# Optimization experiments

Measured on AMD Instinct MI355X. Metric: run time of the kernel, lower is better.

Reference implementation:

```python
import math
import jax, jax.numpy as jnp
import numpy as np

B, T, C, FD, K, V = 8, 2048, 256, 256, 128, 256

def setup_inputs() -> dict:
    key = jax.random.key(0)
    ks = jax.random.split(key, 8)
    s = 0.02
    return {
        "inp": jax.random.normal(ks[0], (B, T, C), jnp.float32),
        "feature": jax.random.normal(ks[1], (B, T, FD), jnp.float32),
        "Wq": jax.random.normal(ks[2], (C + FD, K), jnp.float32) * s,
        "bq": jnp.zeros((K,), jnp.float32),
        "Wk": jax.random.normal(ks[3], (C, K), jnp.float32) * s,
        "bk": jnp.zeros((K,), jnp.float32),
        "Wv": jax.random.normal(ks[4], (C, V), jnp.float32) * s,
        "bv": jnp.zeros((V,), jnp.float32),
    }

def reference(inp, feature, Wq, bq, Wk, bk, Wv, bv):
    # inp: [B,T,C], feature: [B,T,FD]
    t = inp.shape[1]
    q = jnp.concatenate([inp, feature], axis=-1) @ Wq + bq   # [B,T,K]
    k = inp @ Wk + bk                                        # [B,T,K]
    v = inp @ Wv + bv                                        # [B,T,V]
    # scores[b, j, i] = q_j . k_i ; original masks where i > j (strict upper tri)
    scores = jnp.einsum('bjk,bik->bji', q, k)                # [B,T,T]
    mask = jnp.triu(jnp.ones((t, t), dtype=bool), k=1)       # mask[j,i] = i > j
    scores = jnp.where(mask[None], -jnp.inf, scores) / math.sqrt(K)
    # NOTE: original softmax is over dim=1 (the query/row axis), not the key axis
    attn = jax.nn.softmax(scores, axis=1)                    # [B,T,T]
    out = jnp.einsum('bji,biv->bjv', attn, v)                # [B,T,V]
    return jnp.concatenate([inp, out], axis=-1)              # [B,T,C+V]
```

## Files before the change

kernel.cpp:

```cpp
#include <hip/hip_runtime.h>
#include <hip/hip_bf16.h>
#include <cstdint>

#define Bb  8
#define Tt  2048
#define Cc  256
#define FDd 256
#define Kk  128
#define Vv  256
#define BT  (Bb * Tt)
#define NTRI 136

#define INV_SQRT_K 0.08838834764831845f

typedef __bf16 bf16x8 __attribute__((ext_vector_type(8)));
typedef __bf16 bf16x4 __attribute__((ext_vector_type(4)));
typedef float  f32x4  __attribute__((ext_vector_type(4)));

__device__ __forceinline__ void gload16(const void* g, void* l) {
  __builtin_amdgcn_global_load_lds(
      (const __attribute__((address_space(1))) void*)g,
      (__attribute__((address_space(3))) void*)l, 16, 0, 0);
}

__global__ __launch_bounds__(256) void prepw_kernel(
    const float4* __restrict__ inp4, const float4* __restrict__ feat4,
    float4* __restrict__ out4, bf16x4* __restrict__ inpB4,
    bf16x4* __restrict__ featB4,
    const float* __restrict__ Wq, const float* __restrict__ Wk,
    const float* __restrict__ Wv, __bf16* __restrict__ Wqt,
    __bf16* __restrict__ Wkt, __bf16* __restrict__ Wvt)
{
  if (blockIdx.x < 4096) {
    const int g = blockIdx.x * 256 + threadIdx.x;
    const int row = g >> 6, c = g & 63;
    const float4 x = inp4[g];
    out4[(size_t)row * 128 + c] = x;
    bf16x4 xb; xb[0] = (__bf16)x.x; xb[1] = (__bf16)x.y; xb[2] = (__bf16)x.z; xb[3] = (__bf16)x.w;
    inpB4[g] = xb;
    const float4 f = feat4[g];
    bf16x4 fb; fb[0] = (__bf16)f.x; fb[1] = (__bf16)f.y; fb[2] = (__bf16)f.z; fb[3] = (__bf16)f.w;
    featB4[g] = fb;
  } else {
    const int g = (blockIdx.x - 4096) * 256 + threadIdx.x;
    if (g < 65536) {
      const int n = g >> 9, k = g & 511;
      Wqt[g] = (__bf16)Wq[k * 128 + n];
    } else if (g < 98304) {
      const int h = g - 65536;
      const int n = h >> 8, k = h & 255;
      Wkt[h] = (__bf16)Wk[k * 128 + n];
    } else {
      const int h = g - 98304;
      const int n = h >> 8, k = h & 255;
      Wvt[h] = (__bf16)Wv[k * 256 + n];
    }
  }
}

__global__ __launch_bounds__(256, 3) void qkv_mfma_kernel(
    const __bf16* __restrict__ inpB, const __bf16* __restrict__ featB,
    const __bf16* __restrict__ Wqt, const __bf16* __restrict__ Wkt,
    const __bf16* __restrict__ Wvt,
    const float* __restrict__ bq, const float* __restrict__ bk,
    const float* __restrict__ bv,
    __bf16* __restrict__ qb, __bf16* __restrict__ kb, __bf16* __restrict__ vT)
{
  __shared__ __bf16 Atile[128 * 64];
  __shared__ __bf16 Btile[128 * 64];
  const int panel = blockIdx.y;
  const int m0 = blockIdx.x * 128;
  const int lane = threadIdx.x & 63, wave = threadIdx.x >> 6;
  const int cl = lane & 15, quad = lane >> 4;
  const int jl0 = (wave >> 1) * 64;
  const int vl0 = (wave & 1) * 64;

  const __bf16* Wt; const float* bias; int kblocks;
  if (panel == 0)      { Wt = Wqt; bias = bq; kblocks = 8; }
  else if (panel == 1) { Wt = Wkt; bias = bk; kblocks = 4; }
  else                 { Wt = Wvt + (size_t)(panel - 2) * 128 * 256;
                         bias = bv + (panel - 2) * 128; kblocks = 4; }
  const int Kd = kblocks * 64;

  const int lrow = lane >> 3;
  const int lchunk = ((lane & 7) ^ lrow) * 8;

  f32x4 acc[4][4];
#pragma unroll
  for (int mt = 0; mt < 4; ++mt)
#pragma unroll
    for (int nt = 0; nt < 4; ++nt) acc[mt][nt] = (f32x4){0.f, 0.f, 0.f, 0.f};

  for (int kb = 0; kb < kblocks; ++kb) {
    const __bf16* Asrc = (panel == 0 && kb >= 4) ? featB : inpB;
    const int koff = (panel == 0 && kb >= 4) ? (kb - 4) * 64 : kb * 64;
    __syncthreads();
#pragma unroll
    for (int t = 0; t < 4; ++t) {
      const int r0 = wave * 32 + t * 8;
      gload16(Asrc + (size_t)(m0 + r0 + lrow) * 256 + koff + lchunk, Atile + r0 * 64);
      gload16(Wt + (size_t)(r0 + lrow) * Kd + kb * 64 + lchunk, Btile + r0 * 64);
    }
    __syncthreads();
#pragma unroll
    for (int ks = 0; ks < 2; ++ks) {
      bf16x8 af[4], bfr[4];
#pragma unroll
      for (int mt = 0; mt < 4; ++mt) {
        const int jlr = jl0 + mt * 16 + cl;
        af[mt] = *(const bf16x8*)(Atile + jlr * 64 + (((ks * 4 + quad) ^ (jlr & 7)) * 8));
      }
#pragma unroll
      for (int nt = 0; nt < 4; ++nt) {
        const int vlr = vl0 + nt * 16 + cl;
        bfr[nt] = *(const bf16x8*)(Btile + vlr * 64 + (((ks * 4 + quad) ^ (vlr & 7)) * 8));
      }
#pragma unroll
      for (int mt = 0; mt < 4; ++mt)
#pragma unroll
        for (int nt = 0; nt < 4; ++nt)
          acc[mt][nt] = __builtin_amdgcn_mfma_f32_16x16x32_bf16(af[mt], bfr[nt], acc[mt][nt], 0, 0, 0);
    }
  }

  if (panel < 2) {
    __bf16* dst = (panel == 0) ? qb : kb;
    const float scale = (panel == 0) ? INV_SQRT_K : 1.0f;
#pragma unroll
    for (int mt = 0; mt < 4; ++mt) {
      const int row = m0 + jl0 + mt * 16 + quad * 4;
#pragma unroll
      for (int nt = 0; nt < 4; ++nt) {
        const int col = vl0 + nt * 16 + cl;
        const float bs = bias[col];
#pragma unroll
        for (int r = 0; r < 4; ++r)
          dst[(size_t)(row + r) * Kk + col] = (__bf16)((acc[mt][nt][r] + bs) * scale);
      }
    }
  } else {
    const int b = m0 >> 11;
#pragma unroll
    for (int mt = 0; mt < 4; ++mt) {
      const int t0 = (m0 & (Tt - 1)) + jl0 + mt * 16 + quad * 4;
#pragma unroll
      for (int nt = 0; nt < 4; ++nt) {
        const int vcol = (panel - 2) * 128 + vl0 + nt * 16 + cl;
        const float bs = bias[vl0 + nt * 16 + cl];
        bf16x4 v4;
#pragma unroll
        for (int r = 0; r < 4; ++r) v4[r] = (__bf16)(acc[mt][nt][r] + bs);
        *(bf16x4*)(vT + (size_t)(b * Vv + vcol) * Tt + t0) = v4;
      }
    }
  }
}

__global__ __launch_bounds__(256, 2) void sexp_kernel(
    const __bf16* __restrict__ qb, const __bf16* __restrict__ kb,
    __bf16* __restrict__ expS, float* __restrict__ partialD)
{
  __shared__ __bf16 tiles[2 * 128 * 128];
  __shared__ float lcs[4][64];
  __bf16* Qtile = tiles;
  __bf16* Ktile = tiles + 128 * 128;
  float*  P     = (float*)tiles;

  const int b = blockIdx.x, l = blockIdx.y;
  int jt = 0, base = 0;
  while (base + jt + 1 <= l) { base += jt + 1; ++jt; }
  const int it = l - base;

  const int lane = threadIdx.x & 63, wave = threadIdx.x >> 6;
  const int cl = lane & 15, quad = lane >> 4;
  const int jl0 = (wave >> 1) * 64;
  const int il0 = (wave & 1) * 64;
  const size_t rowbase = (size_t)b * Tt;

  {
    const int srow = lane >> 4;
    const int cslot = lane & 15;
    const __bf16* qsrc = qb + (rowbase + jt * 128) * Kk;
    const __bf16* ksrc = kb + (rowbase + it * 128) * Kk;
#pragma unroll
    for (int t = 0; t < 8; ++t) {
      const int r0 = wave * 32 + t * 4;
      const int row = r0 + srow;
      const int cg = (cslot ^ (row & 7)) * 8;
      gload16(qsrc + (size_t)row * Kk + cg, Qtile + r0 * 128);
      gload16(ksrc + (size_t)row * Kk + cg, Ktile + r0 * 128);
    }
  }
  __syncthreads();

  f32x4 acc[4][4];
#pragma unroll
  for (int mt = 0; mt < 4; ++mt)
#pragma unroll
    for (int nt = 0; nt < 4; ++nt) acc[mt][nt] = (f32x4){0.f, 0.f, 0.f, 0.f};

#pragma unroll
  for (int s = 0; s < 4; ++s) {
    bf16x8 af[4], bfr[4];
#pragma unroll
    for (int mt = 0; mt < 4; ++mt) {
      const int jlr = jl0 + mt * 16 + cl;
      af[mt] = *(const bf16x8*)(Qtile + jlr * 128 + (((s * 4 + quad) ^ (jlr & 7)) * 8));
    }
#pragma unroll
    for (int nt = 0; nt < 4; ++nt) {
      const int ilr = il0 + nt * 16 + cl;
      bfr[nt] = *(const bf16x8*)(Ktile + ilr * 128 + (((s * 4 + quad) ^ (ilr & 7)) * 8));
    }
#pragma unroll
    for (int mt = 0; mt < 4; ++mt)
#pragma unroll
      for (int nt = 0; nt < 4; ++nt)
        acc[mt][nt] = __builtin_amdgcn_mfma_f32_16x16x32_bf16(af[mt], bfr[nt], acc[mt][nt], 0, 0, 0);
  }
  __syncthreads();

  const bool diag = (it == jt);
  float cs[4] = {0.f, 0.f, 0.f, 0.f};
#pragma unroll
  for (int mt = 0; mt < 4; ++mt) {
    const int jl = jl0 + mt * 16 + quad * 4;
#pragma unroll
    for (int nt = 0; nt < 4; ++nt) {
      const int il = il0 + nt * 16 + cl;
#pragma unroll
      for (int r = 0; r < 4; ++r) {
        float p = __expf(acc[mt][nt][r]);
        if (diag && il > (jl + r)) p = 0.f;
        cs[nt] += (float)(__bf16)p;
        const int row = jl + r;
        P[row * 128 + (il ^ (((row >> 2) & 1) << 4))] = p;
      }
    }
  }
#pragma unroll
  for (int nt = 0; nt < 4; ++nt) {
    cs[nt] += __shfl_xor(cs[nt], 16);
    cs[nt] += __shfl_xor(cs[nt], 32);
  }
  if (quad == 0) {
#pragma unroll
    for (int nt = 0; nt < 4; ++nt) lcs[wave][nt * 16 + cl] = cs[nt];
  }
  __syncthreads();

  __bf16* slot = expS + ((size_t)(b * NTRI + l)) * (128 * 128);
  {
    const int srow = lane >> 4;
    const int c0 = (lane & 15) * 8;
#pragma unroll
    for (int t = 0; t < 8; ++t) {
      const int row = wave * 32 + t * 4 + srow;
      const int c0p = c0 ^ (((row >> 2) & 1) << 4);
      const f32x4 p0 = *(const f32x4*)(P + row * 128 + c0p);
      const f32x4 p1 = *(const f32x4*)(P + row * 128 + c0p + 4);
      bf16x8 pb;
#pragma unroll
      for (int u = 0; u < 4; ++u) { pb[u] = (__bf16)p0[u]; pb[4 + u] = (__bf16)p1[u]; }
      *(bf16x8*)(slot + (size_t)row * 128 + c0) = pb;
    }
  }

  const int tid = threadIdx.x;
  if (tid < 128) {
    const int w0 = (tid < 64) ? 0 : 1;
    const int lc = tid & 63;
    const float s = lcs[w0][lc] + lcs[w0 + 2][lc];
    partialD[((size_t)b * 16 + jt) * Tt + it * 128 + tid] = s;
  }
}

__global__ __launch_bounds__(256) void dvscale_kernel(
    const float* __restrict__ partialD, bf16x8* __restrict__ vT8)
{
  __shared__ float rec[32];
  const int b = blockIdx.x, ic = blockIdx.y;
  const int i0 = ic * 32;
  const int tid = threadIdx.x;
  if (tid < 32) {
    const int i = i0 + tid;
    float s = 0.f;
#pragma unroll
    for (int jt = 0; jt < 16; ++jt) s += partialD[((size_t)b * 16 + jt) * Tt + i];
    rec[tid] = 1.0f / s;
  }
  __syncthreads();
  const int iu = tid & 3, v0 = tid >> 2;
#pragma unroll
  for (int p = 0; p < 4; ++p) {
    const int v = v0 + p * 64;
    const size_t idx = ((size_t)b * Vv + v) * (Tt / 8) + (i0 >> 3) + iu;
    bf16x8 x = vT8[idx];
    const int rb = iu * 8;
#pragma unroll
    for (int t = 0; t < 8; ++t) x[t] = (__bf16)((float)x[t] * rec[rb + t]);
    vT8[idx] = x;
  }
}

__global__ __launch_bounds__(256, 4) void pvgemm_kernel(
    const __bf16* __restrict__ expS, const __bf16* __restrict__ vT,
    float* __restrict__ out)
{
  __shared__ __bf16 At[2][64 * 64];
  __shared__ __bf16 Bt[2][64 * 64];
  const int b = blockIdx.x;
  const int p = blockIdx.y >> 2;
  const int nq = blockIdx.y & 3;
  const int lane = threadIdx.x & 63, wave = threadIdx.x >> 6;
  const int cl = lane & 15, quad = lane >> 4;
  const int jl0 = (wave >> 1) * 32;
  const int vl0 = (wave & 1) * 32;
  const int lrow = lane >> 3;
  const int lchunk = ((lane & 7) ^ lrow) * 8;
  const __bf16* vbase = vT + ((size_t)b * Vv + nq * 64) * Tt;

#pragma unroll
  for (int sp = 0; sp < 2; ++sp) {
    const int jt64 = sp ? p : 31 - p;
    const int jt128 = jt64 >> 1;
    const int rowoff = (jt64 & 1) * 64;
    const int ksteps = jt64 + 1;
    const size_t tribase = (size_t)(b * NTRI + (jt128 * (jt128 + 1)) / 2) * 16384;

    f32x4 acc[2][2];
#pragma unroll
    for (int mt = 0; mt < 2; ++mt)
#pragma unroll
      for (int nt = 0; nt < 2; ++nt) acc[mt][nt] = (f32x4){0.f, 0.f, 0.f, 0.f};

#pragma unroll
    for (int t = 0; t < 2; ++t) {
      const int r0 = wave * 16 + t * 8;
      gload16(expS + tribase + (size_t)(rowoff + r0 + lrow) * 128 + lchunk,
              At[0] + r0 * 64);
      gload16(vbase + (size_t)(r0 + lrow) * Tt + lchunk, Bt[0] + r0 * 64);
    }
    __syncthreads();

    int buf = 0;
    for (int kb = 0; kb < ksteps; ++kb) {
      if (kb + 1 < ksteps) {
        const int kn = kb + 1;
        const __bf16* Ag = expS + tribase + (size_t)(kn >> 1) * 16384
                         + (size_t)rowoff * 128 + (kn & 1) * 64;
        const int i0n = kn * 64;
#pragma unroll
        for (int t = 0; t < 2; ++t) {
          const int r0 = wave * 16 + t * 8;
          gload16(Ag + (size_t)(r0 + lrow) * 128 + lchunk, At[buf ^ 1] + r0 * 64);
          gload16(vbase + (size_t)(r0 + lrow) * Tt + i0n + lchunk, Bt[buf ^ 1] + r0 * 64);
        }
      }
#pragma unroll
      for (int ks = 0; ks < 2; ++ks) {
        bf16x8 af[2], bfr[2];
#pragma unroll
        for (int mt = 0; mt < 2; ++mt) {
          const int jlr = jl0 + mt * 16 + cl;
          af[mt] = *(const bf16x8*)(At[buf] + jlr * 64 + (((ks * 4 + quad) ^ (jlr & 7)) * 8));
        }
#pragma unroll
        for (int nt = 0; nt < 2; ++nt) {
          const int vlr = vl0 + nt * 16 + cl;
          bfr[nt] = *(const bf16x8*)(Bt[buf] + vlr * 64 + (((ks * 4 + quad) ^ (vlr & 7)) * 8));
        }
#pragma unroll
        for (int mt = 0; mt < 2; ++mt)
#pragma unroll
          for (int nt = 0; nt < 2; ++nt)
            acc[mt][nt] = __builtin_amdgcn_mfma_f32_16x16x32_bf16(af[mt], bfr[nt], acc[mt][nt], 0, 0, 0);
      }
      __syncthreads();
      buf ^= 1;
    }

    float* orow = out + ((size_t)b * Tt + jt64 * 64 + jl0) * (size_t)(Cc + Vv)
                + Cc + nq * 64 + vl0;
#pragma unroll
    for (int mt = 0; mt < 2; ++mt)
#pragma unroll
      for (int nt = 0; nt < 2; ++nt)
#pragma unroll
        for (int r = 0; r < 4; ++r)
          orow[(size_t)(mt * 16 + quad * 4 + r) * (Cc + Vv) + nt * 16 + cl] = acc[mt][nt][r];

    __syncthreads();
  }
}

extern "C" void kernel_launch(void* const* d_in, const int* in_sizes, int n_in,
                              void* d_out, int out_size, void* d_ws, size_t ws_size,
                              hipStream_t stream) {
  const float* inp  = (const float*)d_in[0];
  const float* feat = (const float*)d_in[1];
  const float* Wq   = (const float*)d_in[2];
  const float* bq   = (const float*)d_in[3];
  const float* Wk   = (const float*)d_in[4];
  const float* bk   = (const float*)d_in[5];
  const float* Wv   = (const float*)d_in[6];
  const float* bv   = (const float*)d_in[7];
  float* out = (float*)d_out;

  char* ws = (char*)d_ws;
  __bf16* inpB   = (__bf16*)(ws);
  __bf16* featB  = (__bf16*)(ws + (8u << 20));
  __bf16* qb     = (__bf16*)(ws + (16u << 20));
  __bf16* kb     = (__bf16*)(ws + (20u << 20));
  __bf16* vT     = (__bf16*)(ws + (24u << 20));
  __bf16* Wqt    = (__bf16*)(ws + (32u << 20));
  __bf16* Wkt    = (__bf16*)(ws + (32u << 20) + (128u << 10));
  __bf16* Wvt    = (__bf16*)(ws + (32u << 20) + (192u << 10));
  float*  partialD = (float*)(ws + (33u << 20));
  __bf16* expS     = (__bf16*)(ws + (36u << 20));

  prepw_kernel<<<dim3(4096 + 640), 256, 0, stream>>>(
      (const float4*)inp, (const float4*)feat, (float4*)out,
      (bf16x4*)inpB, (bf16x4*)featB, Wq, Wk, Wv, Wqt, Wkt, Wvt);
  qkv_mfma_kernel<<<dim3(BT / 128, 4), 256, 0, stream>>>(
      inpB, featB, Wqt, Wkt, Wvt, bq, bk, bv, qb, kb, vT);
  sexp_kernel<<<dim3(Bb, NTRI), 256, 0, stream>>>(qb, kb, expS, partialD);
  dvscale_kernel<<<dim3(Bb, 64), 256, 0, stream>>>(partialD, (bf16x8*)vT);
  pvgemm_kernel<<<dim3(Bb, 64), 256, 0, stream>>>(expS, vT, out);
}
```

Baseline: 157.0 us.

## Double-buffer QKV GEMM tiles and split paired PV tiles into separate blocks

The QKV projection kernel now double-buffers its A and B tiles in LDS, prefetching the next k-block while the MFMAs run on the current one. Its launch bound drops from 3 to 2 blocks per SM to make room for the doubled LDS. The PV GEMM no longer pairs a long and a short triangular row tile in one block; each block handles one 64-row tile, the grid doubles to 128 in y, and blocks are ordered longest-first. This is meant to hide global-load latency and raise parallelism, at the cost of lower occupancy in QKV and load imbalance handled by the scheduler instead of by pairing.

```diff
diff --git a/kernel.cpp b/kernel.cpp
--- a/kernel.cpp
+++ b/kernel.cpp
@@ -58,7 +58,7 @@
   }
 }
 
-__global__ __launch_bounds__(256, 3) void qkv_mfma_kernel(
+__global__ __launch_bounds__(256, 2) void qkv_mfma_kernel(
     const __bf16* __restrict__ inpB, const __bf16* __restrict__ featB,
     const __bf16* __restrict__ Wqt, const __bf16* __restrict__ Wkt,
     const __bf16* __restrict__ Wvt,
@@ -66,8 +66,8 @@
     const float* __restrict__ bv,
     __bf16* __restrict__ qb, __bf16* __restrict__ kb, __bf16* __restrict__ vT)
 {
-  __shared__ __bf16 Atile[128 * 64];
-  __shared__ __bf16 Btile[128 * 64];
+  __shared__ __bf16 At[2][128 * 64];
+  __shared__ __bf16 Bt[2][128 * 64];
   const int panel = blockIdx.y;
   const int m0 = blockIdx.x * 128;
   const int lane = threadIdx.x & 63, wave = threadIdx.x >> 6;
@@ -91,29 +91,42 @@
 #pragma unroll
     for (int nt = 0; nt < 4; ++nt) acc[mt][nt] = (f32x4){0.f, 0.f, 0.f, 0.f};
 
-  for (int kb = 0; kb < kblocks; ++kb) {
-    const __bf16* Asrc = (panel == 0 && kb >= 4) ? featB : inpB;
-    const int koff = (panel == 0 && kb >= 4) ? (kb - 4) * 64 : kb * 64;
-    __syncthreads();
+  {
+    const __bf16* Asrc = inpB;
 #pragma unroll
     for (int t = 0; t < 4; ++t) {
       const int r0 = wave * 32 + t * 8;
-      gload16(Asrc + (size_t)(m0 + r0 + lrow) * 256 + koff + lchunk, Atile + r0 * 64);
-      gload16(Wt + (size_t)(r0 + lrow) * Kd + kb * 64 + lchunk, Btile + r0 * 64);
-    }
-    __syncthreads();
+      gload16(Asrc + (size_t)(m0 + r0 + lrow) * 256 + lchunk, At[0] + r0 * 64);
+      gload16(Wt + (size_t)(r0 + lrow) * Kd + lchunk, Bt[0] + r0 * 64);
+    }
+  }
+  __syncthreads();
+
+  int buf = 0;
+  for (int kb = 0; kb < kblocks; ++kb) {
+    if (kb + 1 < kblocks) {
+      const int kn = kb + 1;
+      const __bf16* Asrc = (panel == 0 && kn >= 4) ? featB : inpB;
+      const int koff = (panel == 0 && kn >= 4) ? (kn - 4) * 64 : kn * 64;
+#pragma unroll
+      for (int t = 0; t < 4; ++t) {
+        const int r0 = wave * 32 + t * 8;
+        gload16(Asrc + (size_t)(m0 + r0 + lrow) * 256 + koff + lchunk, At[buf ^ 1] + r0 * 64);
+        gload16(Wt + (size_t)(r0 + lrow) * Kd + kn * 64 + lchunk, Bt[buf ^ 1] + r0 * 64);
+      }
+    }
 #pragma unroll
     for (int ks = 0; ks < 2; ++ks) {
       bf16x8 af[4], bfr[4];
 #pragma unroll
       for (int mt = 0; mt < 4; ++mt) {
         const int jlr = jl0 + mt * 16 + cl;
-        af[mt] = *(const bf16x8*)(Atile + jlr * 64 + (((ks * 4 + quad) ^ (jlr & 7)) * 8));
+        af[mt] = *(const bf16x8*)(At[buf] + jlr * 64 + (((ks * 4 + quad) ^ (jlr & 7)) * 8));
       }
 #pragma unroll
       for (int nt = 0; nt < 4; ++nt) {
         const int vlr = vl0 + nt * 16 + cl;
-        bfr[nt] = *(const bf16x8*)(Btile + vlr * 64 + (((ks * 4 + quad) ^ (vlr & 7)) * 8));
+        bfr[nt] = *(const bf16x8*)(Bt[buf] + vlr * 64 + (((ks * 4 + quad) ^ (vlr & 7)) * 8));
       }
 #pragma unroll
       for (int mt = 0; mt < 4; ++mt)
@@ -121,6 +134,8 @@
         for (int nt = 0; nt < 4; ++nt)
           acc[mt][nt] = __builtin_amdgcn_mfma_f32_16x16x32_bf16(af[mt], bfr[nt], acc[mt][nt], 0, 0, 0);
     }
+    __syncthreads();
+    buf ^= 1;
   }
 
   if (panel < 2) {
@@ -310,8 +325,9 @@
   __shared__ __bf16 At[2][64 * 64];
   __shared__ __bf16 Bt[2][64 * 64];
   const int b = blockIdx.x;
-  const int p = blockIdx.y >> 2;
-  const int nq = blockIdx.y & 3;
+  const int y = (int)blockIdx.y;
+  const int jt64 = 31 - (y >> 2);
+  const int nq = y & 3;
   const int lane = threadIdx.x & 63, wave = threadIdx.x >> 6;
   const int cl = lane & 15, quad = lane >> 4;
   const int jl0 = (wave >> 1) * 32;
@@ -320,78 +336,72 @@
   const int lchunk = ((lane & 7) ^ lrow) * 8;
   const __bf16* vbase = vT + ((size_t)b * Vv + nq * 64) * Tt;
 
-#pragma unroll
-  for (int sp = 0; sp < 2; ++sp) {
-    const int jt64 = sp ? p : 31 - p;
-    const int jt128 = jt64 >> 1;
-    const int rowoff = (jt64 & 1) * 64;
-    const int ksteps = jt64 + 1;
-    const size_t tribase = (size_t)(b * NTRI + (jt128 * (jt128 + 1)) / 2) * 16384;
-
-    f32x4 acc[2][2];
-#pragma unroll
-    for (int mt = 0; mt < 2; ++mt)
-#pragma unroll
-      for (int nt = 0; nt < 2; ++nt) acc[mt][nt] = (f32x4){0.f, 0.f, 0.f, 0.f};
-
-#pragma unroll
-    for (int t = 0; t < 2; ++t) {
-      const int r0 = wave * 16 + t * 8;
-      gload16(expS + tribase + (size_t)(rowoff + r0 + lrow) * 128 + lchunk,
-              At[0] + r0 * 64);
-      gload16(vbase + (size_t)(r0 + lrow) * Tt + lchunk, Bt[0] + r0 * 64);
+  const int jt128 = jt64 >> 1;
+  const int rowoff = (jt64 & 1) * 64;
+  const int ksteps = jt64 + 1;
+  const size_t tribase = (size_t)(b * NTRI + (jt128 * (jt128 + 1)) / 2) * 16384;
+
+  f32x4 acc[2][2];
+#pragma unroll
+  for (int mt = 0; mt < 2; ++mt)
+#pragma unroll
+    for (int nt = 0; nt < 2; ++nt) acc[mt][nt] = (f32x4){0.f, 0.f, 0.f, 0.f};
+
+#pragma unroll
+  for (int t = 0; t < 2; ++t) {
+    const int r0 = wave * 16 + t * 8;
+    gload16(expS + tribase + (size_t)(rowoff + r0 + lrow) * 128 + lchunk,
+            At[0] + r0 * 64);
+    gload16(vbase + (size_t)(r0 + lrow) * Tt + lchunk, Bt[0] + r0 * 64);
+  }
+  __syncthreads();
+
+  int buf = 0;
+  for (int kb = 0; kb < ksteps; ++kb) {
+    if (kb + 1 < ksteps) {
+      const int kn = kb + 1;
+      const __bf16* Ag = expS + tribase + (size_t)(kn >> 1) * 16384
+                       + (size_t)rowoff * 128 + (kn & 1) * 64;
+      const int i0n = kn * 64;
+#pragma unroll
+      for (int t = 0; t < 2; ++t) {
+        const int r0 = wave * 16 + t * 8;
+        gload16(Ag + (size_t)(r0 + lrow) * 128 + lchunk, At[buf ^ 1] + r0 * 64);
+        gload16(vbase + (size_t)(r0 + lrow) * Tt + i0n + lchunk, Bt[buf ^ 1] + r0 * 64);
+      }
+    }
+#pragma unroll
+    for (int ks = 0; ks < 2; ++ks) {
+      bf16x8 af[2], bfr[2];
+#pragma unroll
+      for (int mt = 0; mt < 2; ++mt) {
+        const int jlr = jl0 + mt * 16 + cl;
+        af[mt] = *(const bf16x8*)(At[buf] + jlr * 64 + (((ks * 4 + quad) ^ (jlr & 7)) * 8));
+      }
+#pragma unroll
+      for (int nt = 0; nt < 2; ++nt) {
+        const int vlr = vl0 + nt * 16 + cl;
+        bfr[nt] = *(const bf16x8*)(Bt[buf] + vlr * 64 + (((ks * 4 + quad) ^ (vlr & 7)) * 8));
+      }
+#pragma unroll
+      for (int mt = 0; mt < 2; ++mt)
+#pragma unroll
+        for (int nt = 0; nt < 2; ++nt)
+          acc[mt][nt] = __builtin_amdgcn_mfma_f32_16x16x32_bf16(af[mt], bfr[nt], acc[mt][nt], 0, 0, 0);
     }
     __syncthreads();
-
-    int buf = 0;
-    for (int kb = 0; kb < ksteps; ++kb) {
-      if (kb + 1 < ksteps) {
-        const int kn = kb + 1;
-        const __bf16* Ag = expS + tribase + (size_t)(kn >> 1) * 16384
-                         + (size_t)rowoff * 128 + (kn & 1) * 64;
-        const int i0n = kn * 64;
-#pragma unroll
-        for (int t = 0; t < 2; ++t) {
-          const int r0 = wave * 16 + t * 8;
-          gload16(Ag + (size_t)(r0 + lrow) * 128 + lchunk, At[buf ^ 1] + r0 * 64);
-          gload16(vbase + (size_t)(r0 + lrow) * Tt + i0n + lchunk, Bt[buf ^ 1] + r0 * 64);
-        }
-      }
-#pragma unroll
-      for (int ks = 0; ks < 2; ++ks) {
-        bf16x8 af[2], bfr[2];
-#pragma unroll
-        for (int mt = 0; mt < 2; ++mt) {
-          const int jlr = jl0 + mt * 16 + cl;
-          af[mt] = *(const bf16x8*)(At[buf] + jlr * 64 + (((ks * 4 + quad) ^ (jlr & 7)) * 8));
-        }
-#pragma unroll
-        for (int nt = 0; nt < 2; ++nt) {
-          const int vlr = vl0 + nt * 16 + cl;
-          bfr[nt] = *(const bf16x8*)(Bt[buf] + vlr * 64 + (((ks * 4 + quad) ^ (vlr & 7)) * 8));
-        }
-#pragma unroll
-        for (int mt = 0; mt < 2; ++mt)
-#pragma unroll
-          for (int nt = 0; nt < 2; ++nt)
-            acc[mt][nt] = __builtin_amdgcn_mfma_f32_16x16x32_bf16(af[mt], bfr[nt], acc[mt][nt], 0, 0, 0);
-      }
-      __syncthreads();
-      buf ^= 1;
-    }
-
-    float* orow = out + ((size_t)b * Tt + jt64 * 64 + jl0) * (size_t)(Cc + Vv)
-                + Cc + nq * 64 + vl0;
-#pragma unroll
-    for (int mt = 0; mt < 2; ++mt)
-#pragma unroll
-      for (int nt = 0; nt < 2; ++nt)
-#pragma unroll
-        for (int r = 0; r < 4; ++r)
-          orow[(size_t)(mt * 16 + quad * 4 + r) * (Cc + Vv) + nt * 16 + cl] = acc[mt][nt][r];
-
-    __syncthreads();
-  }
+    buf ^= 1;
+  }
+
+  float* orow = out + ((size_t)b * Tt + jt64 * 64 + jl0) * (size_t)(Cc + Vv)
+              + Cc + nq * 64 + vl0;
+#pragma unroll
+  for (int mt = 0; mt < 2; ++mt)
+#pragma unroll
+    for (int nt = 0; nt < 2; ++nt)
+#pragma unroll
+      for (int r = 0; r < 4; ++r)
+        orow[(size_t)(mt * 16 + quad * 4 + r) * (Cc + Vv) + nt * 16 + cl] = acc[mt][nt][r];
 }
 
 extern "C" void kernel_launch(void* const* d_in, const int* in_sizes, int n_in,
@@ -426,5 +436,5 @@
       inpB, featB, Wqt, Wkt, Wvt, bq, bk, bv, qb, kb, vT);
   sexp_kernel<<<dim3(Bb, NTRI), 256, 0, stream>>>(qb, kb, expS, partialD);
   dvscale_kernel<<<dim3(Bb, 64), 256, 0, stream>>>(partialD, (bf16x8*)vT);
-  pvgemm_kernel<<<dim3(Bb, 64), 256, 0, stream>>>(expS, vT, out);
-}
+  pvgemm_kernel<<<dim3(Bb, 128), 256, 0, stream>>>(expS, vT, out);
+}
```

After: 154.7 us (median of 2 runs). About the same (-1.5%).
